# Kernel tuning notes

Hardware: AMD Instinct MI355X
Metric: run time of the kernel (lower is better)

## Reference

```python
import jax, jax.numpy as jnp
import numpy as np

NUM_EMBEDDINGS = 1024
EMBEDDING_DIM = 64
COMMITMENT_COST = 0.1
DECAY = 0.9
EPSILON = 1e-05


def setup_inputs() -> dict:
    key = jax.random.key(0)
    k1, k2, k3 = jax.random.split(key, 3)
    inputs = jax.random.normal(k1, (16, EMBEDDING_DIM, 4096), dtype=jnp.float32)
    embedding_weight = jax.random.normal(k2, (NUM_EMBEDDINGS, EMBEDDING_DIM), dtype=jnp.float32)
    ema_cluster_size = jnp.zeros((NUM_EMBEDDINGS,), dtype=jnp.float32)
    ema_w = jax.random.normal(k3, (NUM_EMBEDDINGS, EMBEDDING_DIM), dtype=jnp.float32)
    return {
        "inputs": inputs,
        "embedding_weight": embedding_weight,
        "ema_cluster_size": ema_cluster_size,
        "ema_w": ema_w,
    }


def reference(inputs, embedding_weight, ema_cluster_size, ema_w):
    K, D = embedding_weight.shape
    # (B, C, L) -> (B, L, C); C == embedding_dim
    x = jnp.transpose(inputs, (0, 2, 1))
    B, L, _ = x.shape
    flat = x.reshape(-1, D)  # [N, D], N = B*L
    N = flat.shape[0]

    distances = (
        jnp.sum(flat * flat, axis=1, keepdims=True)
        + jnp.sum(embedding_weight * embedding_weight, axis=1)
        - 2.0 * (flat @ embedding_weight.T)
    )
    idx = jnp.argmin(distances, axis=1)  # [N] int

    # embedding lookup (equivalent to one-hot @ weight)
    quantized = embedding_weight[idx].reshape(B, L, D)

    # one-hot column sums and scatter-reduction, without materializing [N, K]
    counts = jnp.zeros((K,), dtype=flat.dtype).at[idx].add(1.0)  # sum(encodings, 0)
    dw = jax.ops.segment_sum(flat, idx, num_segments=K)  # encodings^T @ flat_input

    # EMA updates (training path)
    cs = ema_cluster_size * DECAY + (1.0 - DECAY) * counts
    n = jnp.sum(cs)
    cs = (cs + EPSILON) / (n + K * EPSILON) * n
    new_ema_w = ema_w * DECAY + (1.0 - DECAY) * dw
    new_embedding_weight = new_ema_w / cs[:, None]

    # KLDivLoss(batchmean)(softmax(quantized.detach()), softmax(inputs)) over dim=2
    p_in = jax.nn.softmax(jax.lax.stop_gradient(quantized), axis=2)
    p_tgt = jax.nn.softmax(x, axis=2)
    kl = jnp.sum(p_tgt * (jnp.log(p_tgt) - p_in)) / B
    loss = COMMITMENT_COST * kl

    # straight-through estimator
    quantized_st = x + jax.lax.stop_gradient(quantized - x)

    avg_probs = counts / N
    perplexity = jnp.exp(-jnp.sum(avg_probs * jnp.log(avg_probs + 1e-10)))

    out = jnp.transpose(quantized_st, (0, 2, 1))  # back to (B, C, L)
    encoding_indices = idx[:, None]
    return (out, loss, perplexity, new_embedding_weight, encoding_indices)
```

## Files before the change

### kernel.cpp

```cpp
#include <hip/hip_runtime.h>

#define LDIM 4096
#define DDIM 64
#define KCODES 1024
#define BDIM 16
#define NROWS 65536
#define NSLICE 8
#define SLICE_ROWS (NROWS / NSLICE)

typedef __attribute__((ext_vector_type(8))) short short8;
typedef __attribute__((ext_vector_type(16))) float float16v;

__device__ __forceinline__ unsigned int orderf(float f) {
  unsigned int u = __float_as_uint(f);
  return (u & 0x80000000u) ? ~u : (u | 0x80000000u);
}

__device__ __forceinline__ unsigned long long shfl_xor_u64(unsigned long long v, int m) {
  int lo = __shfl_xor((int)(unsigned int)(v & 0xffffffffull), m, 64);
  int hi = __shfl_xor((int)(unsigned int)(v >> 32), m, 64);
  return ((unsigned long long)(unsigned int)hi << 32) | (unsigned int)lo;
}

__device__ __forceinline__ unsigned int bf16_rne(float x) {
  unsigned int u = __float_as_uint(x);
  return (u + 0x7FFFu + ((u >> 16) & 1u)) >> 16;
}

__global__ void prep_kernel(const float* __restrict__ Ew,
                            float* __restrict__ enorm,
                            float* __restrict__ SE,
                            unsigned short* __restrict__ Epk2) {
  int k = blockIdx.x;
  int d = threadIdx.x;
  float v = Ew[k * DDIM + d];
  float n2 = v * v;
  #pragma unroll
  for (int o = 32; o > 0; o >>= 1) n2 += __shfl_xor(n2, o, 64);
  float m = v;
  #pragma unroll
  for (int o = 32; o > 0; o >>= 1) m = fmaxf(m, __shfl_xor(m, o, 64));
  float e = __expf(v - m);
  float Z = e;
  #pragma unroll
  for (int o = 32; o > 0; o >>= 1) Z += __shfl_xor(Z, o, 64);
  SE[k * DDIM + d] = e / Z;
  if (d == 0) enorm[k] = n2;

  unsigned int rh = bf16_rne(v);
  float hif = __uint_as_float(rh << 16);
  unsigned int rl = bf16_rne(v - hif);
  int tile = k >> 5, mm = k & 31;
  int s = d >> 4, h = (d >> 3) & 1, j = d & 7;
  int base = tile * 4096 + (h * 32 + mm) * 8 + j;
  Epk2[base + s * 512]        = (unsigned short)rh;
  Epk2[base + (4 + s) * 512]  = (unsigned short)rl;
}

__launch_bounds__(256, 2)
__global__ void argmin_kernel(const float* __restrict__ inp,
                              const unsigned short* __restrict__ Epk2,
                              const float* __restrict__ enorm,
                              int* __restrict__ idx_ws,
                              float* __restrict__ outidx) {
  const int tid = threadIdx.x;
  const int lane = tid & 63;
  const int w = tid >> 6;
  const int half = lane >> 5;
  const int m = lane & 31;
  const int row_base = blockIdx.x * 128 + w * 32;
  const int b = row_base >> 12;
  const int l0 = row_base & 4095;
  const float* xp = inp + (size_t)b * DDIM * LDIM + l0 + m;

  short8 afr[8];
  #pragma unroll
  for (int s = 0; s < 4; s++) {
    #pragma unroll
    for (int j = 0; j < 8; j++) {
      int d = 16 * s + 8 * half + j;
      float x = xp[(size_t)d * LDIM];
      unsigned int rh = bf16_rne(x);
      float hif = __uint_as_float(rh << 16);
      unsigned int rl = bf16_rne(x - hif);
      afr[s][j] = (short)(unsigned short)rh;
      afr[4 + s][j] = (short)(unsigned short)rl;
    }
  }

  float bsc[16];
  int bix[16];
  #pragma unroll
  for (int j = 0; j < 16; j++) { bsc[j] = 1e30f; bix[j] = 0; }

  const unsigned short* eb = Epk2 + lane * 8;

  short8 bA[8], bB[8];
  float enA, enB;

  float16v zacc = {};

  #pragma unroll
  for (int s = 0; s < 4; s++) {
    bA[s]     = *(const short8*)(eb + s * 512);
    bA[4 + s] = *(const short8*)(eb + 2048 + s * 512);
  }
  enA = enorm[m];

  #pragma unroll 1
  for (int i = 0; i < 16; i++) {
    const int tB = 2 * i + 1;
    {
      const unsigned short* p = eb + tB * 4096;
      #pragma unroll
      for (int s = 0; s < 4; s++) {
        bB[s]     = *(const short8*)(p + s * 512);
        bB[4 + s] = *(const short8*)(p + 2048 + s * 512);
      }
      enB = enorm[tB * 32 + m];
    }
    {
      float16v acc = __builtin_amdgcn_mfma_f32_32x32x16_bf16(afr[0], bA[0], zacc, 0, 0, 0);
      acc = __builtin_amdgcn_mfma_f32_32x32x16_bf16(afr[0], bA[4], acc, 0, 0, 0);
      acc = __builtin_amdgcn_mfma_f32_32x32x16_bf16(afr[4], bA[0], acc, 0, 0, 0);
      #pragma unroll
      for (int s = 1; s < 4; s++) {
        acc = __builtin_amdgcn_mfma_f32_32x32x16_bf16(afr[s], bA[s], acc, 0, 0, 0);
        acc = __builtin_amdgcn_mfma_f32_32x32x16_bf16(afr[s], bA[4 + s], acc, 0, 0, 0);
        acc = __builtin_amdgcn_mfma_f32_32x32x16_bf16(afr[4 + s], bA[s], acc, 0, 0, 0);
      }
      int ci = 2 * i * 32 + m;
      #pragma unroll
      for (int j = 0; j < 16; j++) {
        float sc = fmaf(-2.f, acc[j], enA);
        if (sc < bsc[j]) { bsc[j] = sc; bix[j] = ci; }
      }
    }
    if (i < 15) {
      const unsigned short* p = eb + (2 * i + 2) * 4096;
      #pragma unroll
      for (int s = 0; s < 4; s++) {
        bA[s]     = *(const short8*)(p + s * 512);
        bA[4 + s] = *(const short8*)(p + 2048 + s * 512);
      }
      enA = enorm[(2 * i + 2) * 32 + m];
    }
    {
      float16v acc = __builtin_amdgcn_mfma_f32_32x32x16_bf16(afr[0], bB[0], zacc, 0, 0, 0);
      acc = __builtin_amdgcn_mfma_f32_32x32x16_bf16(afr[0], bB[4], acc, 0, 0, 0);
      acc = __builtin_amdgcn_mfma_f32_32x32x16_bf16(afr[4], bB[0], acc, 0, 0, 0);
      #pragma unroll
      for (int s = 1; s < 4; s++) {
        acc = __builtin_amdgcn_mfma_f32_32x32x16_bf16(afr[s], bB[s], acc, 0, 0, 0);
        acc = __builtin_amdgcn_mfma_f32_32x32x16_bf16(afr[s], bB[4 + s], acc, 0, 0, 0);
        acc = __builtin_amdgcn_mfma_f32_32x32x16_bf16(afr[4 + s], bB[s], acc, 0, 0, 0);
      }
      int ci = tB * 32 + m;
      #pragma unroll
      for (int j = 0; j < 16; j++) {
        float sc = fmaf(-2.f, acc[j], enB);
        if (sc < bsc[j]) { bsc[j] = sc; bix[j] = ci; }
      }
    }
  }

  #pragma unroll
  for (int j = 0; j < 16; j++) {
    unsigned long long key =
        ((unsigned long long)orderf(bsc[j]) << 32) | (unsigned int)bix[j];
    #pragma unroll
    for (int mm = 1; mm < 32; mm <<= 1) {
      unsigned long long o = shfl_xor_u64(key, mm);
      if (o < key) key = o;
    }
    if (m == 0) {
      int row_local = (j & 3) + 8 * (j >> 2) + 4 * half;
      int grow = row_base + row_local;
      int cidx = (int)(key & 0xffffffffull);
      idx_ws[grow] = cidx;
      outidx[grow] = (float)cidx;
    }
  }
}

__launch_bounds__(256)
__global__ void outkl_dw_kernel(const float* __restrict__ inp,
                                const float* __restrict__ Ew,
                                const float* __restrict__ SE,
                                const int* __restrict__ idx_ws,
                                float* __restrict__ out,
                                float* __restrict__ klacc,
                                float* __restrict__ partial,
                                float* __restrict__ pcounts) {
  __shared__ float smem[11528];
  const int tid = threadIdx.x;

  if (blockIdx.x < 512) {
    float* dwp = smem;
    float* cnt = smem + KCODES;
    const int d = blockIdx.x & 63;
    const int slice = blockIdx.x >> 6;
    const bool do_cnt = (d == 0);

    #pragma unroll
    for (int i = 0; i < KCODES / 256; i++) {
      dwp[tid + i * 256] = 0.f;
      cnt[tid + i * 256] = 0.f;
    }
    __syncthreads();

    const int r0 = slice * SLICE_ROWS;
    for (int i = tid; i < SLICE_ROWS; i += 256) {
      int r = r0 + i;
      int b = r >> 12, l = r & 4095;
      float x = inp[(size_t)b * DDIM * LDIM + (size_t)d * LDIM + l];
      int k = idx_ws[r];
      atomicAdd(&dwp[k], x);
      if (do_cnt) atomicAdd(&cnt[k], 1.0f);
    }
    __syncthreads();

    float* dst = partial + ((size_t)slice * 64 + d) * KCODES;
    #pragma unroll
    for (int i = 0; i < KCODES / 256; i++) dst[tid + i * 256] = dwp[tid + i * 256];
    if (do_cnt) {
      float* cd = pcounts + (size_t)slice * KCODES;
      #pragma unroll
      for (int i = 0; i < KCODES / 256; i++) cd[tid + i * 256] = cnt[tid + i * 256];
    }
  } else {
    int*   kk  = (int*)smem;
    float* Et  = smem + 256;
    float* Qt  = smem + 4352;
    float* Zp  = smem + 8448;
    float* S1p = smem + 9472;
    float* Up  = smem + 10496;
    float* red4 = smem + 11520;

    const int obid = blockIdx.x - 512;
    const int r0 = obid * 256;
    const int b = r0 >> 12;
    const int l0 = r0 & 4095;
    const float* xbase = inp + (size_t)b * DDIM * LDIM + l0;
    float* obase = out + (size_t)b * DDIM * LDIM + l0;
    const int w = tid >> 6, lane = tid & 63;

    kk[tid] = idx_ws[r0 + tid];
    __syncthreads();
    const int myk = kk[tid];
    const int gi = ((tid & 3) << 6) | (tid >> 2);

    float Zc[4] = {0.f, 0.f, 0.f, 0.f};
    float S1c[4] = {0.f, 0.f, 0.f, 0.f};
    float Uc[4] = {0.f, 0.f, 0.f, 0.f};

    #pragma unroll 1
    for (int c = 0; c < 4; c++) {
      {
        const float4* Ep = (const float4*)(Ew + myk * DDIM + c * 16);
        const float4* Qp = (const float4*)(SE + myk * DDIM + c * 16);
        #pragma unroll
        for (int q = 0; q < 4; q++) {
          float4 ev = Ep[q], qv = Qp[q];
          Et[(4 * q + 0) * 256 + tid] = ev.x;
          Et[(4 * q + 1) * 256 + tid] = ev.y;
          Et[(4 * q + 2) * 256 + tid] = ev.z;
          Et[(4 * q + 3) * 256 + tid] = ev.w;
          Qt[(4 * q + 0) * 256 + gi] = qv.x;
          Qt[(4 * q + 1) * 256 + gi] = qv.y;
          Qt[(4 * q + 2) * 256 + gi] = qv.z;
          Qt[(4 * q + 3) * 256 + gi] = qv.w;
        }
      }
      __syncthreads();
      #pragma unroll
      for (int t = 0; t < 4; t++) {
        const int dq = 4 * w + t;
        const int d = c * 16 + dq;
        float4 xv = *(const float4*)(xbase + (size_t)d * LDIM + lane * 4);
        float4 ov = *(const float4*)&Et[dq * 256 + lane * 4];
        *(float4*)(obase + (size_t)d * LDIM + lane * 4) = ov;
        #pragma unroll
        for (int j = 0; j < 4; j++) {
          float x = (j == 0) ? xv.x : (j == 1) ? xv.y : (j == 2) ? xv.z : xv.w;
          float e = __expf(x);
          Zc[j] += e;
          S1c[j] += e * x;
          Uc[j] += e * Qt[dq * 256 + (j << 6) + lane];
        }
      }
      __syncthreads();
    }

    #pragma unroll
    for (int j = 0; j < 4; j++) {
      Zp[w * 256 + 4 * lane + j] = Zc[j];
      S1p[w * 256 + 4 * lane + j] = S1c[j];
      Up[w * 256 + 4 * lane + j] = Uc[j];
    }
    __syncthreads();
    float Z = 0.f, S1 = 0.f, U = 0.f;
    #pragma unroll
    for (int w2 = 0; w2 < 4; w2++) {
      Z += Zp[w2 * 256 + tid];
      S1 += S1p[w2 * 256 + tid];
      U += Up[w2 * 256 + tid];
    }
    float kl = (S1 - U) / Z - __logf(Z);
    #pragma unroll
    for (int o = 32; o > 0; o >>= 1) kl += __shfl_xor(kl, o, 64);
    if (lane == 0) red4[w] = kl;
    __syncthreads();
    if (tid == 0)
      atomicAdd(klacc, red4[0] + red4[1] + red4[2] + red4[3]);
  }
}

__launch_bounds__(256)
__global__ void finalize_kernel(const float* __restrict__ partial,
                                const float* __restrict__ pcounts,
                                const float* __restrict__ emaw,
                                const float* __restrict__ emacs,
                                const float* __restrict__ klacc,
                                float* __restrict__ emb_out,
                                float* __restrict__ loss_out,
                                float* __restrict__ perp_out) {
  __shared__ float red[4], red2[4];
  const int tid = threadIdx.x;
  const int i = blockIdx.x * 256 + tid;
  const int k = i >> 6, d = i & 63;

  float se = 0.f;
  #pragma unroll
  for (int t = 0; t < 4; t++) se += emacs[tid * 4 + t];
  #pragma unroll
  for (int o = 32; o > 0; o >>= 1) se += __shfl_xor(se, o, 64);
  if ((tid & 63) == 0) red[tid >> 6] = se;
  __syncthreads();
  const float S = red[0] + red[1] + red[2] + red[3];
  const float N = 0.9f * S + 0.1f * (float)NROWS;

  float c = 0.f;
  #pragma unroll
  for (int sl = 0; sl < NSLICE; sl++) c += pcounts[sl * KCODES + k];
  float cs = fmaf(0.1f, c, emacs[k] * 0.9f);
  float csp = (cs + 1e-5f) / (N + (float)KCODES * 1e-5f) * N;

  float s = 0.f;
  #pragma unroll
  for (int sl = 0; sl < NSLICE; sl++)
    s += partial[((size_t)sl * 64 + d) * KCODES + k];
  emb_out[i] = fmaf(0.1f, s, emaw[i] * 0.9f) / csp;

  if (blockIdx.x == 0) {
    float es = 0.f;
    #pragma unroll
    for (int t = 0; t < 4; t++) {
      int kk = tid * 4 + t;
      float cc = 0.f;
      #pragma unroll
      for (int sl = 0; sl < NSLICE; sl++) cc += pcounts[sl * KCODES + kk];
      float a = cc * (1.0f / (float)NROWS);
      es += a * logf(a + 1e-10f);
    }
    #pragma unroll
    for (int o = 32; o > 0; o >>= 1) es += __shfl_xor(es, o, 64);
    if ((tid & 63) == 0) red2[tid >> 6] = es;
    __syncthreads();
    if (tid == 0) {
      *perp_out = expf(-(red2[0] + red2[1] + red2[2] + red2[3]));
      *loss_out = 0.1f * (*klacc) * (1.0f / 16.0f);
    }
  }
}

extern "C" void kernel_launch(void* const* d_in, const int* in_sizes, int n_in,
                              void* d_out, int out_size, void* d_ws, size_t ws_size,
                              hipStream_t stream) {
  const float* inp   = (const float*)d_in[0];
  const float* Ew    = (const float*)d_in[1];
  const float* emacs = (const float*)d_in[2];
  const float* emaw  = (const float*)d_in[3];

  float* out      = (float*)d_out;
  float* loss_out = out + 4194304;
  float* perp_out = out + 4194305;
  float* emb_out  = out + 4194306;
  float* idxf_out = out + 4194306 + 65536;

  char* ws = (char*)d_ws;
  int*   idx_ws  = (int*)(ws);
  float* klacc   = (float*)(ws + 262144);
  float* enorm   = (float*)(ws + 266496);
  float* SE      = (float*)(ws + 274688);
  unsigned short* Epk2 = (unsigned short*)(ws + 536832);
  float* partial = (float*)(ws + 536832);
  float* pcounts = (float*)(ws + 2633984);

  hipMemsetAsync(ws + 262144, 0, 256, stream);

  prep_kernel<<<KCODES, 64, 0, stream>>>(Ew, enorm, SE, Epk2);
  argmin_kernel<<<512, 256, 0, stream>>>(inp, Epk2, enorm, idx_ws, idxf_out);
  outkl_dw_kernel<<<768, 256, 0, stream>>>(inp, Ew, SE, idx_ws, out, klacc,
                                           partial, pcounts);
  finalize_kernel<<<NROWS / 256, 256, 0, stream>>>(partial, pcounts, emaw, emacs,
                                                   klacc, emb_out, loss_out,
                                                   perp_out);
}
```

Measured before the change: 165.4 us.

## Fuse output gather and KL loss into argmin kernel; vectorize dw scatter

The argmin kernel now computes softmax statistics (exp, Z, S1) while loading inputs, redistributes the winning index to per-row lanes via shuffles, then gathers the codebook row to write the output and accumulate the KL term with one atomic per wave. This removes a second full read of the input and the idx round-trip for the output/KL path. The dw scatter moves into its own kernel that uses float4/int4 loads. The cost is higher register pressure in the argmin kernel, which holds 32 exp values, plus strided scalar output stores and one global atomic per wave on klacc.

```diff
diff --git a/kernel.cpp b/kernel.cpp
--- a/kernel.cpp
+++ b/kernel.cpp
@@ -58,11 +58,15 @@
 }
 
 __launch_bounds__(256, 2)
-__global__ void argmin_kernel(const float* __restrict__ inp,
-                              const unsigned short* __restrict__ Epk2,
-                              const float* __restrict__ enorm,
-                              int* __restrict__ idx_ws,
-                              float* __restrict__ outidx) {
+__global__ void argmin_fused_kernel(const float* __restrict__ inp,
+                                    const unsigned short* __restrict__ Epk2,
+                                    const float* __restrict__ enorm,
+                                    const float* __restrict__ SE,
+                                    const float* __restrict__ Ew,
+                                    int* __restrict__ idx_ws,
+                                    float* __restrict__ outidx,
+                                    float* __restrict__ out,
+                                    float* __restrict__ klacc) {
   const int tid = threadIdx.x;
   const int lane = tid & 63;
   const int w = tid >> 6;
@@ -74,12 +78,18 @@
   const float* xp = inp + (size_t)b * DDIM * LDIM + l0 + m;
 
   short8 afr[8];
+  float ex[4][8];
+  float Zp = 0.f, S1p = 0.f;
   #pragma unroll
   for (int s = 0; s < 4; s++) {
     #pragma unroll
     for (int j = 0; j < 8; j++) {
       int d = 16 * s + 8 * half + j;
       float x = xp[(size_t)d * LDIM];
+      float e = __expf(x);
+      ex[s][j] = e;
+      Zp += e;
+      S1p = fmaf(e, x, S1p);
       unsigned int rh = bf16_rne(x);
       float hif = __uint_as_float(rh << 16);
       unsigned int rl = bf16_rne(x - hif);
@@ -164,6 +174,10 @@
     }
   }
 
+  const int jr = (m & 3) | ((m >> 3) << 2);
+  const int hr = (m >> 2) & 1;
+  unsigned long long mykey = 0ull;
+
   #pragma unroll
   for (int j = 0; j < 16; j++) {
     unsigned long long key =
@@ -173,146 +187,100 @@
       unsigned long long o = shfl_xor_u64(key, mm);
       if (o < key) key = o;
     }
-    if (m == 0) {
-      int row_local = (j & 3) + 8 * (j >> 2) + 4 * half;
-      int grow = row_base + row_local;
-      int cidx = (int)(key & 0xffffffffull);
-      idx_ws[grow] = cidx;
-      outidx[grow] = (float)cidx;
-    }
-  }
+    if (j == jr) mykey = key;
+  }
+  unsigned long long partner = shfl_xor_u64(mykey, 32);
+  unsigned long long keyrow = (hr == half) ? mykey : partner;
+  const int kr = (int)(keyrow & 0xffffffffull);
+
+  if (half == 0) {
+    idx_ws[row_base + m] = kr;
+    outidx[row_base + m] = (float)kr;
+  }
+
+  float Up = 0.f;
+  const float* sebase = SE + kr * DDIM + 8 * half;
+  const float* ewbase = Ew + kr * DDIM + 8 * half;
+  float* obase = out + (size_t)b * DDIM * LDIM + l0 + m;
+  #pragma unroll
+  for (int s = 0; s < 4; s++) {
+    float4 q0 = *(const float4*)(sebase + 16 * s);
+    float4 q1 = *(const float4*)(sebase + 16 * s + 4);
+    Up = fmaf(ex[s][0], q0.x, Up); Up = fmaf(ex[s][1], q0.y, Up);
+    Up = fmaf(ex[s][2], q0.z, Up); Up = fmaf(ex[s][3], q0.w, Up);
+    Up = fmaf(ex[s][4], q1.x, Up); Up = fmaf(ex[s][5], q1.y, Up);
+    Up = fmaf(ex[s][6], q1.z, Up); Up = fmaf(ex[s][7], q1.w, Up);
+    float4 e0 = *(const float4*)(ewbase + 16 * s);
+    float4 e1 = *(const float4*)(ewbase + 16 * s + 4);
+    const int d0 = 16 * s + 8 * half;
+    obase[(size_t)(d0 + 0) * LDIM] = e0.x;
+    obase[(size_t)(d0 + 1) * LDIM] = e0.y;
+    obase[(size_t)(d0 + 2) * LDIM] = e0.z;
+    obase[(size_t)(d0 + 3) * LDIM] = e0.w;
+    obase[(size_t)(d0 + 4) * LDIM] = e1.x;
+    obase[(size_t)(d0 + 5) * LDIM] = e1.y;
+    obase[(size_t)(d0 + 6) * LDIM] = e1.z;
+    obase[(size_t)(d0 + 7) * LDIM] = e1.w;
+  }
+
+  float Z = Zp + __shfl_xor(Zp, 32, 64);
+  float S1 = S1p + __shfl_xor(S1p, 32, 64);
+  float U = Up + __shfl_xor(Up, 32, 64);
+  float kl = (S1 - U) / Z - __logf(Z);
+  kl = (half == 0) ? kl : 0.f;
+  #pragma unroll
+  for (int o = 1; o < 64; o <<= 1) kl += __shfl_xor(kl, o, 64);
+  if (lane == 0) atomicAdd(klacc, kl);
 }
 
 __launch_bounds__(256)
-__global__ void outkl_dw_kernel(const float* __restrict__ inp,
-                                const float* __restrict__ Ew,
-                                const float* __restrict__ SE,
-                                const int* __restrict__ idx_ws,
-                                float* __restrict__ out,
-                                float* __restrict__ klacc,
-                                float* __restrict__ partial,
-                                float* __restrict__ pcounts) {
-  __shared__ float smem[11528];
+__global__ void dw_kernel(const float* __restrict__ inp,
+                          const int* __restrict__ idx_ws,
+                          float* __restrict__ partial,
+                          float* __restrict__ pcounts) {
+  __shared__ float dwp[KCODES];
+  __shared__ float cnt[KCODES];
   const int tid = threadIdx.x;
-
-  if (blockIdx.x < 512) {
-    float* dwp = smem;
-    float* cnt = smem + KCODES;
-    const int d = blockIdx.x & 63;
-    const int slice = blockIdx.x >> 6;
-    const bool do_cnt = (d == 0);
-
-    #pragma unroll
-    for (int i = 0; i < KCODES / 256; i++) {
-      dwp[tid + i * 256] = 0.f;
-      cnt[tid + i * 256] = 0.f;
-    }
-    __syncthreads();
-
-    const int r0 = slice * SLICE_ROWS;
-    for (int i = tid; i < SLICE_ROWS; i += 256) {
-      int r = r0 + i;
-      int b = r >> 12, l = r & 4095;
-      float x = inp[(size_t)b * DDIM * LDIM + (size_t)d * LDIM + l];
-      int k = idx_ws[r];
-      atomicAdd(&dwp[k], x);
-      if (do_cnt) atomicAdd(&cnt[k], 1.0f);
-    }
-    __syncthreads();
-
-    float* dst = partial + ((size_t)slice * 64 + d) * KCODES;
-    #pragma unroll
-    for (int i = 0; i < KCODES / 256; i++) dst[tid + i * 256] = dwp[tid + i * 256];
+  const int d = blockIdx.x & 63;
+  const int slice = blockIdx.x >> 6;
+  const bool do_cnt = (d == 0);
+
+  #pragma unroll
+  for (int i = 0; i < KCODES / 256; i++) {
+    dwp[tid + i * 256] = 0.f;
+    cnt[tid + i * 256] = 0.f;
+  }
+  __syncthreads();
+
+  const int r0 = slice * SLICE_ROWS;
+  #pragma unroll 1
+  for (int j = 0; j < 8; j++) {
+    const int rbase = r0 + j * 1024 + tid * 4;
+    const int bb = rbase >> 12;
+    const int ll = rbase & 4095;
+    const float4 xv = *(const float4*)(inp + (size_t)bb * DDIM * LDIM +
+                                       (size_t)d * LDIM + ll);
+    const int4 kv = *(const int4*)(idx_ws + rbase);
+    atomicAdd(&dwp[kv.x], xv.x);
+    atomicAdd(&dwp[kv.y], xv.y);
+    atomicAdd(&dwp[kv.z], xv.z);
+    atomicAdd(&dwp[kv.w], xv.w);
     if (do_cnt) {
-      float* cd = pcounts + (size_t)slice * KCODES;
-      #pragma unroll
-      for (int i = 0; i < KCODES / 256; i++) cd[tid + i * 256] = cnt[tid + i * 256];
-    }
-  } else {
-    int*   kk  = (int*)smem;
-    float* Et  = smem + 256;
-    float* Qt  = smem + 4352;
-    float* Zp  = smem + 8448;
-    float* S1p = smem + 9472;
-    float* Up  = smem + 10496;
-    float* red4 = smem + 11520;
-
-    const int obid = blockIdx.x - 512;
-    const int r0 = obid * 256;
-    const int b = r0 >> 12;
-    const int l0 = r0 & 4095;
-    const float* xbase = inp + (size_t)b * DDIM * LDIM + l0;
-    float* obase = out + (size_t)b * DDIM * LDIM + l0;
-    const int w = tid >> 6, lane = tid & 63;
-
-    kk[tid] = idx_ws[r0 + tid];
-    __syncthreads();
-    const int myk = kk[tid];
-    const int gi = ((tid & 3) << 6) | (tid >> 2);
-
-    float Zc[4] = {0.f, 0.f, 0.f, 0.f};
-    float S1c[4] = {0.f, 0.f, 0.f, 0.f};
-    float Uc[4] = {0.f, 0.f, 0.f, 0.f};
-
-    #pragma unroll 1
-    for (int c = 0; c < 4; c++) {
-      {
-        const float4* Ep = (const float4*)(Ew + myk * DDIM + c * 16);
-        const float4* Qp = (const float4*)(SE + myk * DDIM + c * 16);
-        #pragma unroll
-        for (int q = 0; q < 4; q++) {
-          float4 ev = Ep[q], qv = Qp[q];
-          Et[(4 * q + 0) * 256 + tid] = ev.x;
-          Et[(4 * q + 1) * 256 + tid] = ev.y;
-          Et[(4 * q + 2) * 256 + tid] = ev.z;
-          Et[(4 * q + 3) * 256 + tid] = ev.w;
-          Qt[(4 * q + 0) * 256 + gi] = qv.x;
-          Qt[(4 * q + 1) * 256 + gi] = qv.y;
-          Qt[(4 * q + 2) * 256 + gi] = qv.z;
-          Qt[(4 * q + 3) * 256 + gi] = qv.w;
-        }
-      }
-      __syncthreads();
-      #pragma unroll
-      for (int t = 0; t < 4; t++) {
-        const int dq = 4 * w + t;
-        const int d = c * 16 + dq;
-        float4 xv = *(const float4*)(xbase + (size_t)d * LDIM + lane * 4);
-        float4 ov = *(const float4*)&Et[dq * 256 + lane * 4];
-        *(float4*)(obase + (size_t)d * LDIM + lane * 4) = ov;
-        #pragma unroll
-        for (int j = 0; j < 4; j++) {
-          float x = (j == 0) ? xv.x : (j == 1) ? xv.y : (j == 2) ? xv.z : xv.w;
-          float e = __expf(x);
-          Zc[j] += e;
-          S1c[j] += e * x;
-          Uc[j] += e * Qt[dq * 256 + (j << 6) + lane];
-        }
-      }
-      __syncthreads();
-    }
-
-    #pragma unroll
-    for (int j = 0; j < 4; j++) {
-      Zp[w * 256 + 4 * lane + j] = Zc[j];
-      S1p[w * 256 + 4 * lane + j] = S1c[j];
-      Up[w * 256 + 4 * lane + j] = Uc[j];
-    }
-    __syncthreads();
-    float Z = 0.f, S1 = 0.f, U = 0.f;
-    #pragma unroll
-    for (int w2 = 0; w2 < 4; w2++) {
-      Z += Zp[w2 * 256 + tid];
-      S1 += S1p[w2 * 256 + tid];
-      U += Up[w2 * 256 + tid];
-    }
-    float kl = (S1 - U) / Z - __logf(Z);
-    #pragma unroll
-    for (int o = 32; o > 0; o >>= 1) kl += __shfl_xor(kl, o, 64);
-    if (lane == 0) red4[w] = kl;
-    __syncthreads();
-    if (tid == 0)
-      atomicAdd(klacc, red4[0] + red4[1] + red4[2] + red4[3]);
+      atomicAdd(&cnt[kv.x], 1.0f);
+      atomicAdd(&cnt[kv.y], 1.0f);
+      atomicAdd(&cnt[kv.z], 1.0f);
+      atomicAdd(&cnt[kv.w], 1.0f);
+    }
+  }
+  __syncthreads();
+
+  float* dst = partial + ((size_t)slice * 64 + d) * KCODES;
+  #pragma unroll
+  for (int i = 0; i < KCODES / 256; i++) dst[tid + i * 256] = dwp[tid + i * 256];
+  if (do_cnt) {
+    float* cd = pcounts + (size_t)slice * KCODES;
+    #pragma unroll
+    for (int i = 0; i < KCODES / 256; i++) cd[tid + i * 256] = cnt[tid + i * 256];
   }
 }
 
@@ -400,9 +368,9 @@
   hipMemsetAsync(ws + 262144, 0, 256, stream);
 
   prep_kernel<<<KCODES, 64, 0, stream>>>(Ew, enorm, SE, Epk2);
-  argmin_kernel<<<512, 256, 0, stream>>>(inp, Epk2, enorm, idx_ws, idxf_out);
-  outkl_dw_kernel<<<768, 256, 0, stream>>>(inp, Ew, SE, idx_ws, out, klacc,
-                                           partial, pcounts);
+  argmin_fused_kernel<<<512, 256, 0, stream>>>(inp, Epk2, enorm, SE, Ew,
+                                               idx_ws, idxf_out, out, klacc);
+  dw_kernel<<<512, 256, 0, stream>>>(inp, idx_ws, partial, pcounts);
   finalize_kernel<<<NROWS / 256, 256, 0, stream>>>(partial, pcounts, emaw, emacs,
                                                    klacc, emb_out, loss_out,
                                                    perp_out);
```

Measured after the change: 176.0 us. 6.4% more time.
